# Kernel tuning notes

Measured on AMD Instinct MI355X. Metric: run time of the kernel, lower is better.

The kernel has to match this reference:

```python
import jax, jax.numpy as jnp
import numpy as np

V = 50304   # vocab
P = 1024    # max positions
D = 768     # model dim
H = 12      # heads
HD = D // H # head dim (64)
L = 12      # depth
M = 4       # mlp ratio
B = 2
S = 1024
LN_EPS_BLOCK = 1e-6
LN_EPS_FINAL = 1e-5


def setup_inputs() -> dict:
    key = jax.random.key(0)
    ks = jax.random.split(key, 16)
    def n(k, shape, s=0.02):
        return (jax.random.normal(k, shape) * s).astype(jnp.float32)
    inp = {
        'input_ids': jax.random.randint(ks[0], (B, S), 0, V, dtype=jnp.int64) if jax.config.jax_enable_x64 else jax.random.randint(ks[0], (B, S), 0, V).astype(jnp.int32),
        'attention_mask': jnp.ones((B, S), jnp.float32),
        'wte': n(ks[1], (V, D)),
        'wpe': n(ks[2], (P, D)),
        'ln1_g': jnp.ones((L, D), jnp.float32),
        'ln1_b': jnp.zeros((L, D), jnp.float32),
        'qkv_w': n(ks[3], (L, D, 3 * D)),
        'qkv_b': jnp.zeros((L, 3 * D), jnp.float32),
        'proj_w': n(ks[4], (L, D, D)),
        'proj_b': jnp.zeros((L, D), jnp.float32),
        'ln2_g': jnp.ones((L, D), jnp.float32),
        'ln2_b': jnp.zeros((L, D), jnp.float32),
        'fc1_w': n(ks[5], (L, D, M * D)),
        'fc1_b': jnp.zeros((L, M * D), jnp.float32),
        'fc2_w': n(ks[6], (L, M * D, D)),
        'fc2_b': jnp.zeros((L, D), jnp.float32),
        'lnf_g': jnp.ones((D,), jnp.float32),
        'lnf_b': jnp.zeros((D,), jnp.float32),
        'head_b': jnp.zeros((V,), jnp.float32),
    }
    return inp


def _ln(x, g, b, eps):
    mu = jnp.mean(x, -1, keepdims=True)
    var = jnp.mean(jnp.square(x - mu), -1, keepdims=True)
    return (x - mu) * jax.lax.rsqrt(var + eps) * g + b


def _block(x, mask_add, p):
    (g1, b1, wqkv, bqkv, wp, bp, g2, b2, w1, b1m, w2, b2m) = p
    h = _ln(x, g1, b1, LN_EPS_BLOCK)
    qkv = h @ wqkv + bqkv                                  # [B,S,3D]
    qkv = qkv.reshape(x.shape[0], x.shape[1], H, 3 * HD).transpose(0, 2, 1, 3)
    q, k, v = jnp.split(qkv, 3, axis=-1)                   # each [B,H,S,hd]
    scores = jnp.einsum('bhqd,bhkd->bhqk', q, k) / np.float32(np.sqrt(HD))
    causal = jnp.tril(jnp.ones((x.shape[1], x.shape[1]), bool))
    scores = jnp.where(causal, scores, jnp.float32(-10000.0))
    scores = scores + mask_add
    probs = jax.nn.softmax(scores, axis=-1)
    o = jnp.einsum('bhqk,bhkd->bhqd', probs, v)
    o = o.transpose(0, 2, 1, 3).reshape(x.shape[0], x.shape[1], D)
    x = x + (o @ wp + bp)
    h = _ln(x, g2, b2, LN_EPS_BLOCK)
    h = jax.nn.gelu(h @ w1 + b1m, approximate=False)
    x = x + (h @ w2 + b2m)
    return x


def reference(input_ids, attention_mask, wte, wpe, ln1_g, ln1_b, qkv_w, qkv_b,
              proj_w, proj_b, ln2_g, ln2_b, fc1_w, fc1_b, fc2_w, fc2_b,
              lnf_g, lnf_b, head_b):
    seq = input_ids.shape[1]
    mask_add = (1.0 - attention_mask)[:, None, None, :] * jnp.float32(-10000.0)
    x = wte[input_ids] + wpe[jnp.arange(seq)][None]         # [B,S,D]
    layer_params = (ln1_g, ln1_b, qkv_w, qkv_b, proj_w, proj_b,
                    ln2_g, ln2_b, fc1_w, fc1_b, fc2_w, fc2_b)
    def step(h, p):
        return _block(h, mask_add, p), None
    x, _ = jax.lax.scan(step, x, layer_params)
    x = _ln(x, lnf_g, lnf_b, LN_EPS_FINAL)
    logits = x @ wte.T + head_b                             # tied LM head
    return logits
```

## Files before the change

### kernel.cpp

```cpp
#include <hip/hip_runtime.h>
#include <hip/hip_bf16.h>

typedef unsigned short u16;
typedef short bf16x8 __attribute__((ext_vector_type(8)));
typedef float floatx4 __attribute__((ext_vector_type(4)));
typedef u16 u16x4 __attribute__((ext_vector_type(4)));

#define DEV __device__ __forceinline__

DEV u16 f2bf(float f) {
    unsigned u = __builtin_bit_cast(unsigned, f);
    u += 0x7fffu + ((u >> 16) & 1u);
    return (u16)(u >> 16);
}
DEV float bf2f(u16 h) {
    unsigned u = ((unsigned)h) << 16;
    return __builtin_bit_cast(float, u);
}

static constexpr int Dm   = 768;
static constexpr int Hn   = 12;
static constexpr int HDn  = 64;
static constexpr int Ln   = 12;
static constexpr int Vn   = 50304;
static constexpr int Sn   = 1024;
static constexpr int Bn   = 2;
static constexpr int Tn   = Bn * Sn;
static constexpr int DMLP = 4 * Dm;

#define GLOAD_LDS16(gptr, lptr)                                                        \
    __builtin_amdgcn_global_load_lds((const __attribute__((address_space(1))) void*)(gptr), \
                                     (__attribute__((address_space(3))) void*)(lptr), 16, 0, 0)

__global__ __launch_bounds__(256) void k_cvt(const float* __restrict__ s,
                                             u16* __restrict__ d, int n4) {
    int i = blockIdx.x * 256 + threadIdx.x;
    if (i >= n4) return;
    const float4 v = *(const float4*)(s + (size_t)i * 4);
    u16x4 o;
    o[0] = f2bf(v.x); o[1] = f2bf(v.y); o[2] = f2bf(v.z); o[3] = f2bf(v.w);
    *(u16x4*)(d + (size_t)i * 4) = o;
}

__global__ __launch_bounds__(256) void k_tr(const float* __restrict__ src,
                                            u16* __restrict__ dst, int R, int C) {
    __shared__ float tile[32][33];
    const int l = blockIdx.z;
    src += (size_t)l * R * C;
    dst += (size_t)l * R * C;
    const int c0 = blockIdx.x * 32, r0 = blockIdx.y * 32;
    const int tx = threadIdx.x, ty = threadIdx.y;
#pragma unroll
    for (int i = 0; i < 4; i++)
        tile[ty + i * 8][tx] = src[(size_t)(r0 + ty + i * 8) * C + c0 + tx];
    __syncthreads();
#pragma unroll
    for (int i = 0; i < 4; i++)
        dst[(size_t)(c0 + ty + i * 8) * R + r0 + tx] = f2bf(tile[tx][ty + i * 8]);
}

__global__ __launch_bounds__(256) void k_embed(const int* __restrict__ ids,
                                               const float* __restrict__ wte,
                                               const float* __restrict__ wpe,
                                               float* __restrict__ x) {
    int idx = blockIdx.x * 256 + threadIdx.x;
    int t = idx / Dm, d = idx - t * Dm;
    int s = t & (Sn - 1);
    x[idx] = wte[(size_t)ids[t] * Dm + d] + wpe[(size_t)s * Dm + d];
}

__global__ __launch_bounds__(256) void k_ln(const float* __restrict__ x,
                                            const float* __restrict__ g,
                                            const float* __restrict__ bvec,
                                            u16* __restrict__ out, float eps) {
    const int row = blockIdx.x, tid = threadIdx.x;
    const float* xr = x + (size_t)row * Dm;
    float v0 = xr[tid], v1 = xr[tid + 256], v2 = xr[tid + 512];
    float s = v0 + v1 + v2;
    float q = v0 * v0 + v1 * v1 + v2 * v2;
#pragma unroll
    for (int off = 1; off < 64; off <<= 1) {
        s += __shfl_xor(s, off, 64);
        q += __shfl_xor(q, off, 64);
    }
    __shared__ float red[8];
    const int wid = tid >> 6;
    if ((tid & 63) == 0) { red[wid] = s; red[4 + wid] = q; }
    __syncthreads();
    s = red[0] + red[1] + red[2] + red[3];
    q = red[4] + red[5] + red[6] + red[7];
    const float mu  = s * (1.0f / Dm);
    const float var = q * (1.0f / Dm) - mu * mu;
    const float rs  = rsqrtf(var + eps);
    u16* orow = out + (size_t)row * Dm;
    orow[tid]       = f2bf((v0 - mu) * rs * g[tid]       + bvec[tid]);
    orow[tid + 256] = f2bf((v1 - mu) * rs * g[tid + 256] + bvec[tid + 256]);
    orow[tid + 512] = f2bf((v2 - mu) * rs * g[tid + 512] + bvec[tid + 512]);
}

__global__ __launch_bounds__(256) void k_repack(const float* __restrict__ qkv,
                                                u16* __restrict__ q, u16* __restrict__ k,
                                                u16* __restrict__ v) {
    int idx = blockIdx.x * 256 + threadIdx.x;
    int t = idx / (3 * Dm), c = idx - t * (3 * Dm);
    int h = c / 192, rem = c - h * 192;
    int which = rem >> 6, d = rem & 63;
    int b = t >> 10, s = t & (Sn - 1);
    float val = qkv[idx];
    size_t o = ((size_t)(b * Hn + h) * Sn + s) * HDn + d;
    if (which == 0)      q[o] = f2bf(val * 0.125f);
    else if (which == 1) k[o] = f2bf(val);
    else                 v[o] = f2bf(val);
}

template <int MODE>
__global__ __launch_bounds__(256) void k_gemm(const u16* __restrict__ A,
                                              const u16* __restrict__ W,
                                              const float* __restrict__ bias,
                                              const float* __restrict__ resid,
                                              float* __restrict__ outF,
                                              u16* __restrict__ outB,
                                              int M, int N, int K) {
    __shared__ u16 sA[128 * 64];
    __shared__ u16 sW[128 * 64];
    const int tid = threadIdx.x;
    const int lane = tid & 63, wid = tid >> 6;
    const int lane16 = lane & 15, quad = lane >> 4;
    const int m0 = blockIdx.y * 128, n0 = blockIdx.x * 128;
    const int wm = wid & 1, wn = wid >> 1;

    floatx4 acc[4][4];
#pragma unroll
    for (int i = 0; i < 4; i++)
#pragma unroll
        for (int j = 0; j < 4; j++) acc[i][j] = (floatx4){0.f, 0.f, 0.f, 0.f};

    const int KT = K >> 6;
    for (int kt = 0; kt < KT; ++kt) {
        const int kb = kt << 6;
#pragma unroll
        for (int it = 0; it < 4; ++it) {
            int p = it * 256 + tid;
            int row = p >> 3;
            int kc = (p & 7) ^ (row & 7);
            GLOAD_LDS16(A + (size_t)(m0 + row) * K + kb + kc * 8, sA + p * 8);
            GLOAD_LDS16(W + (size_t)(n0 + row) * K + kb + kc * 8, sW + p * 8);
        }
        __syncthreads();
#pragma unroll
        for (int ks = 0; ks < 2; ++ks) {
            bf16x8 af[4], wf[4];
#pragma unroll
            for (int i = 0; i < 4; i++) {
                int m = wm * 64 + i * 16 + lane16;
                int ch = (ks * 4 + quad) ^ (m & 7);
                af[i] = *(const bf16x8*)(sA + m * 64 + ch * 8);
            }
#pragma unroll
            for (int j = 0; j < 4; j++) {
                int n = wn * 64 + j * 16 + lane16;
                int ch = (ks * 4 + quad) ^ (n & 7);
                wf[j] = *(const bf16x8*)(sW + n * 64 + ch * 8);
            }
#pragma unroll
            for (int i = 0; i < 4; i++)
#pragma unroll
                for (int j = 0; j < 4; j++)
                    acc[i][j] = __builtin_amdgcn_mfma_f32_16x16x32_bf16(af[i], wf[j], acc[i][j], 0, 0, 0);
        }
        __syncthreads();
    }

#pragma unroll
    for (int i = 0; i < 4; i++) {
        int rowb = m0 + wm * 64 + i * 16 + quad * 4;
#pragma unroll
        for (int j = 0; j < 4; j++) {
            int col = n0 + wn * 64 + j * 16 + lane16;
            float bc = bias[col];
#pragma unroll
            for (int r = 0; r < 4; r++) {
                size_t off = (size_t)(rowb + r) * N + col;
                float v = acc[i][j][r] + bc;
                if (MODE == 0) {
                    outF[off] = v;
                } else if (MODE == 1) {
                    outF[off] = resid[off] + v;
                } else {
                    float gl = 0.5f * v * (1.0f + erff(v * 0.70710678118654752f));
                    outB[off] = f2bf(gl);
                }
            }
        }
    }
}

__global__ __launch_bounds__(256) void k_attn(const u16* __restrict__ Q,
                                              const u16* __restrict__ Kg,
                                              const u16* __restrict__ Vg,
                                              const float* __restrict__ amask,
                                              u16* __restrict__ out) {
    __shared__ u16 sQ[64 * 72];
    __shared__ u16 sK[64 * 72];
    __shared__ u16 sV[64 * 72];
    __shared__ u16 sP[64 * 72];
    const int tid = threadIdx.x;
    const int lane = tid & 63, wid = tid >> 6;
    const int lane16 = lane & 15, quad = lane >> 4;
    const int blk = blockIdx.x;
    const int qt = blk & 15, bh = blk >> 4;
    const int b = bh / Hn, h = bh - b * Hn;
    const int q0 = qt * 64;
    const u16* Qb = Q + (size_t)bh * Sn * HDn;
    const u16* Kb = Kg + (size_t)bh * Sn * HDn;
    const u16* Vb = Vg + (size_t)bh * Sn * HDn;
    const float* maskb = amask + (size_t)b * Sn;

#pragma unroll
    for (int it = 0; it < 2; ++it) {
        int c = it * 256 + tid;
        int row = c >> 3, kc = c & 7;
        *(bf16x8*)(sQ + row * 72 + kc * 8) = *(const bf16x8*)(Qb + (size_t)(q0 + row) * HDn + kc * 8);
    }

    float mrow[4], lrow[4];
    floatx4 o[4];
#pragma unroll
    for (int r = 0; r < 4; r++) { mrow[r] = -1e30f; lrow[r] = 0.f; }
#pragma unroll
    for (int t = 0; t < 4; t++) o[t] = (floatx4){0.f, 0.f, 0.f, 0.f};

    for (int kt = 0; kt <= qt; ++kt) {
        __syncthreads();
        const int k0 = kt * 64;
#pragma unroll
        for (int it = 0; it < 2; ++it) {
            int c = it * 256 + tid;
            int row = c >> 3, kc = c & 7;
            bf16x8 kv = *(const bf16x8*)(Kb + (size_t)(k0 + row) * HDn + kc * 8);
            *(bf16x8*)(sK + row * 72 + kc * 8) = kv;
            bf16x8 vv = *(const bf16x8*)(Vb + (size_t)(k0 + row) * HDn + kc * 8);
#pragma unroll
            for (int u = 0; u < 8; u++) sV[(kc * 8 + u) * 72 + row] = (u16)vv[u];
        }
        __syncthreads();

        floatx4 s[4];
#pragma unroll
        for (int t = 0; t < 4; t++) s[t] = (floatx4){0.f, 0.f, 0.f, 0.f};
#pragma unroll
        for (int ks = 0; ks < 2; ++ks) {
            bf16x8 aq = *(const bf16x8*)(sQ + (wid * 16 + lane16) * 72 + ks * 32 + quad * 8);
#pragma unroll
            for (int t = 0; t < 4; t++) {
                bf16x8 bk = *(const bf16x8*)(sK + (t * 16 + lane16) * 72 + ks * 32 + quad * 8);
                s[t] = __builtin_amdgcn_mfma_f32_16x16x32_bf16(aq, bk, s[t], 0, 0, 0);
            }
        }

        float madd[4];
#pragma unroll
        for (int t = 0; t < 4; t++)
            madd[t] = (1.0f - maskb[k0 + t * 16 + lane16]) * -10000.0f;
#pragma unroll
        for (int t = 0; t < 4; t++) {
            int kg = k0 + t * 16 + lane16;
#pragma unroll
            for (int r = 0; r < 4; r++) {
                int qg = q0 + wid * 16 + quad * 4 + r;
                float val = s[t][r];
                if (kg > qg) val = -10000.0f;
                s[t][r] = val + madd[t];
            }
        }

        float mnew[4], alpha[4], rsum[4];
#pragma unroll
        for (int r = 0; r < 4; r++) {
            float mx = fmaxf(fmaxf(s[0][r], s[1][r]), fmaxf(s[2][r], s[3][r]));
#pragma unroll
            for (int off = 1; off < 16; off <<= 1) mx = fmaxf(mx, __shfl_xor(mx, off, 64));
            mnew[r] = fmaxf(mrow[r], mx);
            alpha[r] = expf(mrow[r] - mnew[r]);
            rsum[r] = 0.f;
        }
#pragma unroll
        for (int t = 0; t < 4; t++) {
#pragma unroll
            for (int r = 0; r < 4; r++) {
                float p = expf(s[t][r] - mnew[r]);
                rsum[r] += p;
                sP[(wid * 16 + quad * 4 + r) * 72 + t * 16 + lane16] = f2bf(p);
            }
        }
#pragma unroll
        for (int r = 0; r < 4; r++) {
#pragma unroll
            for (int off = 1; off < 16; off <<= 1) rsum[r] += __shfl_xor(rsum[r], off, 64);
            lrow[r] = lrow[r] * alpha[r] + rsum[r];
            mrow[r] = mnew[r];
        }
#pragma unroll
        for (int t = 0; t < 4; t++)
#pragma unroll
            for (int r = 0; r < 4; r++) o[t][r] *= alpha[r];

        __builtin_amdgcn_wave_barrier();

#pragma unroll
        for (int ks = 0; ks < 2; ++ks) {
            bf16x8 ap = *(const bf16x8*)(sP + (wid * 16 + lane16) * 72 + ks * 32 + quad * 8);
#pragma unroll
            for (int t = 0; t < 4; t++) {
                bf16x8 bv = *(const bf16x8*)(sV + (t * 16 + lane16) * 72 + ks * 32 + quad * 8);
                o[t] = __builtin_amdgcn_mfma_f32_16x16x32_bf16(ap, bv, o[t], 0, 0, 0);
            }
        }
    }

#pragma unroll
    for (int t = 0; t < 4; t++) {
#pragma unroll
        for (int r = 0; r < 4; r++) {
            int qg = q0 + wid * 16 + quad * 4 + r;
            float val = o[t][r] / lrow[r];
            out[(size_t)(b * Sn + qg) * Dm + h * HDn + t * 16 + lane16] = f2bf(val);
        }
    }
}

extern "C" void kernel_launch(void* const* d_in, const int* in_sizes, int n_in,
                              void* d_out, int out_size, void* d_ws, size_t ws_size,
                              hipStream_t stream) {
    (void)in_sizes; (void)n_in; (void)out_size; (void)ws_size;

    const int*   ids   = (const int*)  d_in[0];
    const float* amask = (const float*)d_in[1];
    const float* wte   = (const float*)d_in[2];
    const float* wpe   = (const float*)d_in[3];
    const float* ln1g  = (const float*)d_in[4];
    const float* ln1b  = (const float*)d_in[5];
    const float* qkvw  = (const float*)d_in[6];
    const float* qkvb  = (const float*)d_in[7];
    const float* projw = (const float*)d_in[8];
    const float* projb = (const float*)d_in[9];
    const float* ln2g  = (const float*)d_in[10];
    const float* ln2b  = (const float*)d_in[11];
    const float* fc1w  = (const float*)d_in[12];
    const float* fc1b  = (const float*)d_in[13];
    const float* fc2w  = (const float*)d_in[14];
    const float* fc2b  = (const float*)d_in[15];
    const float* lnfg  = (const float*)d_in[16];
    const float* lnfb  = (const float*)d_in[17];
    const float* headb = (const float*)d_in[18];

    char* w = (char*)d_ws;
    u16* wteB = (u16*)w;   w += (size_t)Vn * Dm * 2;
    u16* qkvW = (u16*)w;   w += (size_t)Ln * Dm * 3 * Dm * 2;
    u16* projW = (u16*)w;  w += (size_t)Ln * Dm * Dm * 2;
    u16* fc1W = (u16*)w;   w += (size_t)Ln * Dm * DMLP * 2;
    u16* fc2W = (u16*)w;   w += (size_t)Ln * DMLP * Dm * 2;
    float* x  = (float*)w; w += (size_t)Tn * Dm * 4;
    u16* hbuf = (u16*)w;   w += (size_t)Tn * Dm * 2;
    float* qkv = (float*)w; w += (size_t)Tn * 3 * Dm * 4;
    u16* qb   = (u16*)w;   w += (size_t)Tn * Dm * 2;
    u16* kb   = (u16*)w;   w += (size_t)Tn * Dm * 2;
    u16* vb   = (u16*)w;   w += (size_t)Tn * Dm * 2;
    u16* attn = (u16*)w;   w += (size_t)Tn * Dm * 2;
    u16* mlp  = (u16*)w;   w += (size_t)Tn * DMLP * 2;

    k_cvt<<<(Vn * Dm / 4) / 256, 256, 0, stream>>>(wte, wteB, Vn * Dm / 4);
    dim3 tb(32, 8);
    k_tr<<<dim3(3 * Dm / 32, Dm / 32, Ln), tb, 0, stream>>>(qkvw, qkvW, Dm, 3 * Dm);
    k_tr<<<dim3(Dm / 32, Dm / 32, Ln), tb, 0, stream>>>(projw, projW, Dm, Dm);
    k_tr<<<dim3(DMLP / 32, Dm / 32, Ln), tb, 0, stream>>>(fc1w, fc1W, Dm, DMLP);
    k_tr<<<dim3(Dm / 32, DMLP / 32, Ln), tb, 0, stream>>>(fc2w, fc2W, DMLP, Dm);

    k_embed<<<Tn * Dm / 256, 256, 0, stream>>>(ids, wte, wpe, x);

    for (int l = 0; l < Ln; ++l) {
        k_ln<<<Tn, 256, 0, stream>>>(x, ln1g + l * Dm, ln1b + l * Dm, hbuf, 1e-6f);
        k_gemm<0><<<dim3(3 * Dm / 128, Tn / 128), 256, 0, stream>>>(
            hbuf, qkvW + (size_t)l * 3 * Dm * Dm, qkvb + l * 3 * Dm, nullptr, qkv, nullptr,
            Tn, 3 * Dm, Dm);
        k_repack<<<Tn * 3 * Dm / 256, 256, 0, stream>>>(qkv, qb, kb, vb);
        k_attn<<<Bn * Hn * (Sn / 64), 256, 0, stream>>>(qb, kb, vb, amask, attn);
        k_gemm<1><<<dim3(Dm / 128, Tn / 128), 256, 0, stream>>>(
            attn, projW + (size_t)l * Dm * Dm, projb + l * Dm, x, x, nullptr,
            Tn, Dm, Dm);
        k_ln<<<Tn, 256, 0, stream>>>(x, ln2g + l * Dm, ln2b + l * Dm, hbuf, 1e-6f);
        k_gemm<2><<<dim3(DMLP / 128, Tn / 128), 256, 0, stream>>>(
            hbuf, fc1W + (size_t)l * Dm * DMLP, fc1b + l * DMLP, nullptr, nullptr, mlp,
            Tn, DMLP, Dm);
        k_gemm<1><<<dim3(Dm / 128, Tn / 128), 256, 0, stream>>>(
            mlp, fc2W + (size_t)l * DMLP * Dm, fc2b + l * Dm, x, x, nullptr,
            Tn, Dm, DMLP);
    }

    k_ln<<<Tn, 256, 0, stream>>>(x, lnfg, lnfb, hbuf, 1e-5f);
    k_gemm<0><<<dim3(Vn / 128, Tn / 128), 256, 0, stream>>>(
        hbuf, wteB, headb, nullptr, (float*)d_out, nullptr, Tn, Vn, Dm);
}
```

Baseline: 3.527 ms.

## Fuse QKV repack into GEMM epilogue, split-K atomic residual GEMMs, swizzle blocks

The QKV repack is folded into the GEMM epilogue, which writes scaled bf16 Q/K/V directly in head-major layout. This removes the fp32 qkv buffer and one kernel launch per layer. The proj and fc2 GEMMs become split-K by 4 and atomically add into the residual x, which raises block count for the small N=768 GEMMs at the cost of atomic traffic and nondeterministic summation order. Block IDs are remapped in an XCD-style swizzle with the grid transposed so M varies fastest, aiming for better L2 locality.

```diff
diff --git a/kernel.cpp b/kernel.cpp
--- a/kernel.cpp
+++ b/kernel.cpp
@@ -98,35 +98,25 @@
     orow[tid + 512] = f2bf((v2 - mu) * rs * g[tid + 512] + bvec[tid + 512]);
 }
 
-__global__ __launch_bounds__(256) void k_repack(const float* __restrict__ qkv,
-                                                u16* __restrict__ q, u16* __restrict__ k,
-                                                u16* __restrict__ v) {
-    int idx = blockIdx.x * 256 + threadIdx.x;
-    int t = idx / (3 * Dm), c = idx - t * (3 * Dm);
-    int h = c / 192, rem = c - h * 192;
-    int which = rem >> 6, d = rem & 63;
-    int b = t >> 10, s = t & (Sn - 1);
-    float val = qkv[idx];
-    size_t o = ((size_t)(b * Hn + h) * Sn + s) * HDn + d;
-    if (which == 0)      q[o] = f2bf(val * 0.125f);
-    else if (which == 1) k[o] = f2bf(val);
-    else                 v[o] = f2bf(val);
-}
-
 template <int MODE>
 __global__ __launch_bounds__(256) void k_gemm(const u16* __restrict__ A,
                                               const u16* __restrict__ W,
                                               const float* __restrict__ bias,
-                                              const float* __restrict__ resid,
                                               float* __restrict__ outF,
                                               u16* __restrict__ outB,
+                                              u16* __restrict__ outQ,
+                                              u16* __restrict__ outK,
+                                              u16* __restrict__ outV,
                                               int M, int N, int K) {
     __shared__ u16 sA[128 * 64];
     __shared__ u16 sW[128 * 64];
     const int tid = threadIdx.x;
     const int lane = tid & 63, wid = tid >> 6;
     const int lane16 = lane & 15, quad = lane >> 4;
-    const int m0 = blockIdx.y * 128, n0 = blockIdx.x * 128;
+    const int gx = gridDim.x;
+    int bid = blockIdx.y * gx + blockIdx.x;
+    bid = (bid & 7) * ((gx * gridDim.y) >> 3) + (bid >> 3);
+    const int m0 = (bid % gx) * 128, n0 = (bid / gx) * 128;
     const int wm = wid & 1, wn = wid >> 1;
 
     floatx4 acc[4][4];
@@ -135,9 +125,14 @@
 #pragma unroll
         for (int j = 0; j < 4; j++) acc[i][j] = (floatx4){0.f, 0.f, 0.f, 0.f};
 
-    const int KT = K >> 6;
-    for (int kt = 0; kt < KT; ++kt) {
-        const int kb = kt << 6;
+    int kbeg = 0, kend = K;
+    if (MODE == 4) {
+        const int Kpart = K / (int)gridDim.z;
+        kbeg = blockIdx.z * Kpart;
+        kend = kbeg + Kpart;
+    }
+
+    for (int kb = kbeg; kb < kend; kb += 64) {
 #pragma unroll
         for (int it = 0; it < 4; ++it) {
             int p = it * 256 + tid;
@@ -178,17 +173,33 @@
         for (int j = 0; j < 4; j++) {
             int col = n0 + wn * 64 + j * 16 + lane16;
             float bc = bias[col];
-#pragma unroll
-            for (int r = 0; r < 4; r++) {
-                size_t off = (size_t)(rowb + r) * N + col;
-                float v = acc[i][j][r] + bc;
-                if (MODE == 0) {
-                    outF[off] = v;
-                } else if (MODE == 1) {
-                    outF[off] = resid[off] + v;
-                } else {
-                    float gl = 0.5f * v * (1.0f + erff(v * 0.70710678118654752f));
-                    outB[off] = f2bf(gl);
+            if (MODE == 3) {
+                int h = col / 192, rem = col - h * 192;
+                int which = rem >> 6, d = rem & 63;
+                u16* dst = (which == 0) ? outQ : (which == 1) ? outK : outV;
+                float scale = (which == 0) ? 0.125f : 1.0f;
+#pragma unroll
+                for (int r = 0; r < 4; r++) {
+                    int t = rowb + r;
+                    int b = t >> 10, s = t & (Sn - 1);
+                    size_t o = ((size_t)(b * Hn + h) * Sn + s) * HDn + d;
+                    dst[o] = f2bf((acc[i][j][r] + bc) * scale);
+                }
+            } else {
+#pragma unroll
+                for (int r = 0; r < 4; r++) {
+                    size_t off = (size_t)(rowb + r) * N + col;
+                    if (MODE == 0) {
+                        outF[off] = acc[i][j][r] + bc;
+                    } else if (MODE == 2) {
+                        float v = acc[i][j][r] + bc;
+                        float gl = 0.5f * v * (1.0f + erff(v * 0.70710678118654752f));
+                        outB[off] = f2bf(gl);
+                    } else {
+                        float v = acc[i][j][r];
+                        if (blockIdx.z == 0) v += bc;
+                        atomicAdd(outF + off, v);
+                    }
                 }
             }
         }
@@ -362,7 +373,6 @@
     u16* fc2W = (u16*)w;   w += (size_t)Ln * DMLP * Dm * 2;
     float* x  = (float*)w; w += (size_t)Tn * Dm * 4;
     u16* hbuf = (u16*)w;   w += (size_t)Tn * Dm * 2;
-    float* qkv = (float*)w; w += (size_t)Tn * 3 * Dm * 4;
     u16* qb   = (u16*)w;   w += (size_t)Tn * Dm * 2;
     u16* kb   = (u16*)w;   w += (size_t)Tn * Dm * 2;
     u16* vb   = (u16*)w;   w += (size_t)Tn * Dm * 2;
@@ -380,24 +390,24 @@
 
     for (int l = 0; l < Ln; ++l) {
         k_ln<<<Tn, 256, 0, stream>>>(x, ln1g + l * Dm, ln1b + l * Dm, hbuf, 1e-6f);
-        k_gemm<0><<<dim3(3 * Dm / 128, Tn / 128), 256, 0, stream>>>(
-            hbuf, qkvW + (size_t)l * 3 * Dm * Dm, qkvb + l * 3 * Dm, nullptr, qkv, nullptr,
-            Tn, 3 * Dm, Dm);
-        k_repack<<<Tn * 3 * Dm / 256, 256, 0, stream>>>(qkv, qb, kb, vb);
+        k_gemm<3><<<dim3(Tn / 128, 3 * Dm / 128), 256, 0, stream>>>(
+            hbuf, qkvW + (size_t)l * 3 * Dm * Dm, qkvb + l * 3 * Dm,
+            nullptr, nullptr, qb, kb, vb, Tn, 3 * Dm, Dm);
         k_attn<<<Bn * Hn * (Sn / 64), 256, 0, stream>>>(qb, kb, vb, amask, attn);
-        k_gemm<1><<<dim3(Dm / 128, Tn / 128), 256, 0, stream>>>(
-            attn, projW + (size_t)l * Dm * Dm, projb + l * Dm, x, x, nullptr,
-            Tn, Dm, Dm);
+        k_gemm<4><<<dim3(Tn / 128, Dm / 128, 4), 256, 0, stream>>>(
+            attn, projW + (size_t)l * Dm * Dm, projb + l * Dm,
+            x, nullptr, nullptr, nullptr, nullptr, Tn, Dm, Dm);
         k_ln<<<Tn, 256, 0, stream>>>(x, ln2g + l * Dm, ln2b + l * Dm, hbuf, 1e-6f);
-        k_gemm<2><<<dim3(DMLP / 128, Tn / 128), 256, 0, stream>>>(
-            hbuf, fc1W + (size_t)l * Dm * DMLP, fc1b + l * DMLP, nullptr, nullptr, mlp,
-            Tn, DMLP, Dm);
-        k_gemm<1><<<dim3(Dm / 128, Tn / 128), 256, 0, stream>>>(
-            mlp, fc2W + (size_t)l * DMLP * Dm, fc2b + l * Dm, x, x, nullptr,
-            Tn, Dm, DMLP);
+        k_gemm<2><<<dim3(Tn / 128, DMLP / 128), 256, 0, stream>>>(
+            hbuf, fc1W + (size_t)l * Dm * DMLP, fc1b + l * DMLP,
+            nullptr, mlp, nullptr, nullptr, nullptr, Tn, DMLP, Dm);
+        k_gemm<4><<<dim3(Tn / 128, Dm / 128, 4), 256, 0, stream>>>(
+            mlp, fc2W + (size_t)l * DMLP * Dm, fc2b + l * Dm,
+            x, nullptr, nullptr, nullptr, nullptr, Tn, Dm, DMLP);
     }
 
     k_ln<<<Tn, 256, 0, stream>>>(x, lnfg, lnfb, hbuf, 1e-5f);
-    k_gemm<0><<<dim3(Vn / 128, Tn / 128), 256, 0, stream>>>(
-        hbuf, wteB, headb, nullptr, (float*)d_out, nullptr, Tn, Vn, Dm);
-}
+    k_gemm<0><<<dim3(Tn / 128, Vn / 128), 256, 0, stream>>>(
+        hbuf, wteB, headb, (float*)d_out, nullptr, nullptr, nullptr, nullptr,
+        Tn, Vn, Dm);
+}
```

New measurement: 3.209 ms. 9.0% less time.
